# Performance work log

Measured on AMD Instinct MI355X. Metric: run time of the kernel, lower is better.

Reference implementation:

```python
import jax, jax.numpy as jnp
import numpy as np

N_TREES = 10
N_DEPTH = 8
IN_DIM = 2048
CLASSES = 1000
BATCH = 16384
N_DECISION = 2 ** N_DEPTH - 1          # 255
N_LEAF = 2 ** (N_DEPTH + 1)            # 512 (module's own convention)


def _tiling_pattern():
    # Static gather pattern mapping each (leaf, depth) slot to an index into
    # the packed [decision_p, 1 - decision_p] tensor, exactly as in the source.
    tp = np.zeros((N_LEAF, N_DEPTH), dtype=np.int32)
    dec_idx = 0
    for n in range(N_DEPTH):
        j = 0
        for _ in range(2 ** n):
            rep = 2 ** (N_DEPTH - n)
            tp[j:j + rep, n] = dec_idx
            j += rep
            tp[j:j + rep, n] = N_DECISION + dec_idx
            j += rep
            dec_idx += 1
    return tp.reshape(-1)

FLAT_PATTERN = jnp.asarray(_tiling_pattern())  # [N_LEAF * N_DEPTH]


def setup_inputs() -> dict:
    key = jax.random.key(0)
    kx, kd, kl = jax.random.split(key, 3)
    x = jax.random.normal(kx, (BATCH, IN_DIM), dtype=jnp.float32)
    # small scale so sigmoid logits are not fully saturated (mimics uniform init)
    w_d = jax.random.normal(kd, (N_TREES, IN_DIM, N_DECISION), dtype=jnp.float32) * 0.02
    w_l = jax.random.normal(kl, (N_TREES, N_LEAF, CLASSES), dtype=jnp.float32)
    return {"x": x, "w_d": w_d, "w_l": w_l}


def reference(x, w_d, w_l):
    # decision probabilities for all trees: [T, B, N_DECISION]
    decision_p = jax.nn.sigmoid(jnp.einsum('bi,tid->tbd', x, w_d))
    # packed [p, 1-p]: [T, B, 2*N_DECISION]
    pack = jnp.concatenate([decision_p, 1.0 - decision_p], axis=-1)
    # static gather -> path probability factors: [T, B, N_LEAF, N_DEPTH]
    mu = pack[..., FLAT_PATTERN].reshape(N_TREES, x.shape[0], N_LEAF, N_DEPTH)
    leaf_prob = jnp.prod(mu, axis=-1)               # [T, B, N_LEAF]
    leaf_p = jax.nn.softmax(w_l, axis=-1)           # [T, N_LEAF, C]
    # sum over trees, then average
    return jnp.einsum('tbl,tlc->bc', leaf_prob, leaf_p) / N_TREES
```

## Files before the change

kernel.cpp:

```cpp
#include <hip/hip_runtime.h>
#include <stdint.h>

#define T_TREES 10
#define IN_DIM  2048
#define BATCH   16384
#define CLASSES 1000
#define NDEC    255
#define NPAD    256
#define K2DIM   (T_TREES * NPAD)
#define NPADC   1024

typedef unsigned short u16;
typedef float floatx4 __attribute__((ext_vector_type(4)));
typedef __bf16 bf16x8 __attribute__((ext_vector_type(8)));

__device__ __forceinline__ u16 f2bf(float f) {
    union { float f; uint32_t u; } v; v.f = f;
    uint32_t u = v.u;
    return (u16)((u + 0x7FFFu + ((u >> 16) & 1u)) >> 16);
}
__device__ __forceinline__ float bf2f(u16 h) {
    union { uint32_t u; float f; } v; v.u = ((uint32_t)h) << 16;
    return v.f;
}

__device__ __forceinline__ void gld16(u16* lds_p, const u16* g) {
    __builtin_amdgcn_global_load_lds(
        (__attribute__((address_space(1))) const void*)g,
        (__attribute__((address_space(3))) void*)lds_p,
        16, 0, 0);
}

__global__ __launch_bounds__(256) void cast_x_k(const float4* __restrict__ x,
                                                uint2* __restrict__ xb) {
    int i = blockIdx.x * 256 + threadIdx.x;
    float4 v = x[i];
    uint2 o;
    o.x = (uint32_t)f2bf(v.x) | ((uint32_t)f2bf(v.y) << 16);
    o.y = (uint32_t)f2bf(v.z) | ((uint32_t)f2bf(v.w) << 16);
    xb[i] = o;
}

__global__ void transpose_wd_k(const float* __restrict__ wd, u16* __restrict__ wdT) {
    __shared__ float tile[32][33];
    int tx = threadIdx.x, ty = threadIdx.y;
    int t = blockIdx.z;
    int i0 = blockIdx.x * 32, d0 = blockIdx.y * 32;
#pragma unroll
    for (int r = 0; r < 4; ++r) {
        int i = i0 + ty + r * 8;
        int d = d0 + tx;
        float v = (d < NDEC) ? wd[((size_t)t * IN_DIM + i) * NDEC + d] : 0.0f;
        tile[ty + r * 8][tx] = v;
    }
    __syncthreads();
#pragma unroll
    for (int r = 0; r < 4; ++r) {
        int dd = d0 + ty + r * 8;
        int ii = i0 + tx;
        wdT[((size_t)t * NPAD + dd) * IN_DIM + ii] = f2bf(tile[tx][ty + r * 8]);
    }
}

__global__ __launch_bounds__(256) void softmax_fold_k(const float* __restrict__ wl,
                                                      u16* __restrict__ B2) {
    int wid = threadIdx.x >> 6, lane = threadIdx.x & 63;
    int idx = blockIdx.x * 4 + wid;
    int t = idx >> 8, m = idx & 255;
    const float* r0 = wl + ((size_t)t * 512 + 2 * m) * CLASSES;
    const float* r1 = r0 + CLASSES;
    float v0[16], v1[16];
    float mx0 = -3.0e38f, mx1 = -3.0e38f;
#pragma unroll
    for (int j = 0; j < 16; ++j) {
        int c = lane + 64 * j;
        float a = (c < CLASSES) ? r0[c] : -3.0e38f;
        float b = (c < CLASSES) ? r1[c] : -3.0e38f;
        v0[j] = a; v1[j] = b;
        mx0 = fmaxf(mx0, a); mx1 = fmaxf(mx1, b);
    }
#pragma unroll
    for (int o = 32; o > 0; o >>= 1) {
        mx0 = fmaxf(mx0, __shfl_xor(mx0, o));
        mx1 = fmaxf(mx1, __shfl_xor(mx1, o));
    }
    float s0 = 0.f, s1 = 0.f;
#pragma unroll
    for (int j = 0; j < 16; ++j) {
        int c = lane + 64 * j;
        float e0 = (c < CLASSES) ? __expf(v0[j] - mx0) : 0.f;
        float e1 = (c < CLASSES) ? __expf(v1[j] - mx1) : 0.f;
        v0[j] = e0; v1[j] = e1; s0 += e0; s1 += e1;
    }
#pragma unroll
    for (int o = 32; o > 0; o >>= 1) { s0 += __shfl_xor(s0, o); s1 += __shfl_xor(s1, o); }
    float i0 = 0.1f / s0, i1 = 0.1f / s1;
#pragma unroll
    for (int j = 0; j < 16; ++j) {
        int c = lane + 64 * j;
        float v = (c < CLASSES) ? (v0[j] * i0 + v1[j] * i1) : 0.f;
        B2[(size_t)idx * NPADC + c] = f2bf(v);
    }
}

__global__ void transpose_b2_k(const u16* __restrict__ B2, u16* __restrict__ B2t) {
    __shared__ u16 tile[32][33];
    int tx = threadIdx.x, ty = threadIdx.y;
    int k0 = blockIdx.x * 32, c0 = blockIdx.y * 32;
#pragma unroll
    for (int r = 0; r < 4; ++r)
        tile[ty + r * 8][tx] = B2[(size_t)(k0 + ty + r * 8) * NPADC + c0 + tx];
    __syncthreads();
#pragma unroll
    for (int r = 0; r < 4; ++r)
        B2t[(size_t)(c0 + ty + r * 8) * K2DIM + k0 + tx] = tile[tx][ty + r * 8];
}


#define WAITLGKM_(n) asm volatile("s_waitcnt lgkmcnt(" #n ")" ::: "memory")
#define WAITLGKM(n) WAITLGKM_(n)
#define WAITVM_(n) asm volatile("s_waitcnt vmcnt(" #n ")" ::: "memory")
#define WAITVM(n) WAITVM_(n)
#define SB  __builtin_amdgcn_sched_barrier(0)
#define BAR __builtin_amdgcn_s_barrier()

template<int NT, int EPI>
__global__ __launch_bounds__(512, 2) void gemm8p(const u16* __restrict__ A,
                                                 const u16* __restrict__ B,
                                                 void* __restrict__ Cout) {
    constexpr int K = NT * 64;
    __shared__ __align__(16) u16 lds[8 * 8192];

    const int tid  = threadIdx.x;
    const int wid  = tid >> 6;
    const int lane = tid & 63;
    const int wm = wid >> 2, wn = wid & 3;
    const int quad = lane >> 4, t16 = lane & 15;

    const size_t m0 = (size_t)blockIdx.x * 256;
    const size_t n0 = (size_t)blockIdx.y * 256;
    const u16* __restrict__ Ag = A + m0 * (size_t)K;
    const u16* __restrict__ Bg = B + n0 * (size_t)K;

    const uint32_t stOff = (uint32_t)((wid * 8 + (lane >> 3)) * K)
                         + (uint32_t)(((lane & 7) ^ ((lane >> 3) & 7)) * 8);
    const uint32_t stLds = (uint32_t)(wid * 8 * 64);

#define STAGE(slot, o, tk) do { \
    const u16* gp_ = (((o) < 2) ? Bg : Ag) + ((size_t)(((o) & 1) * 128) * K) \
                   + ((size_t)(tk) * 64) + stOff; \
    gld16(&lds[(slot) * 8192 + stLds], gp_); \
    gld16(&lds[(slot) * 8192 + stLds + 4096], gp_ + (size_t)64 * K); \
  } while (0)

#define AOFF(P, mi, kk) (((P) * 4 + 2 + wm) * 8192 + ((mi) * 16 + t16) * 64 \
                         + ((((kk) * 4 + quad) ^ (t16 & 7)) * 8))
#define BOFF(P, ni, kk) (((P) * 4 + ((wn * 64 + (ni) * 16) >> 7)) * 8192 \
                         + (((wn * 64 + (ni) * 16) & 127) + t16) * 64 \
                         + ((((kk) * 4 + quad) ^ (t16 & 7)) * 8))

#define RD2(dst, P, mi0) do { \
    dst[0][0] = *(const bf16x8*)&lds[AOFF(P, (mi0),     0)]; \
    dst[0][1] = *(const bf16x8*)&lds[AOFF(P, (mi0),     1)]; \
    dst[1][0] = *(const bf16x8*)&lds[AOFF(P, (mi0) + 1, 0)]; \
    dst[1][1] = *(const bf16x8*)&lds[AOFF(P, (mi0) + 1, 1)]; \
  } while (0)

#define RDB(dst, P) do { \
    _Pragma("unroll") \
    for (int ni_ = 0; ni_ < 4; ++ni_) { \
      dst[ni_][0] = *(const bf16x8*)&lds[BOFF(P, ni_, 0)]; \
      dst[ni_][1] = *(const bf16x8*)&lds[BOFF(P, ni_, 1)]; \
    } \
  } while (0)

#define MFQ(p, aq, bs) do { \
    _Pragma("unroll") \
    for (int kk_ = 0; kk_ < 2; ++kk_) { \
      _Pragma("unroll") \
      for (int ni_ = 0; ni_ < 4; ++ni_) { \
        acc[2*(p)][ni_]   = __builtin_amdgcn_mfma_f32_16x16x32_bf16( \
            aq[0][kk_], bs[ni_][kk_], acc[2*(p)][ni_], 0, 0, 0); \
        acc[2*(p)+1][ni_] = __builtin_amdgcn_mfma_f32_16x16x32_bf16( \
            aq[1][kk_], bs[ni_][kk_], acc[2*(p)+1][ni_], 0, 0, 0); \
      } \
    } \
  } while (0)

    floatx4 acc[8][4];
#pragma unroll
    for (int i = 0; i < 8; ++i)
#pragma unroll
        for (int j = 0; j < 4; ++j) acc[i][j] = (floatx4){0.f, 0.f, 0.f, 0.f};

    bf16x8 bA[4][2], bB[4][2];
    bf16x8 a0A[2][2], a0B[2][2];
    bf16x8 aT1[2][2], aT2[2][2], aT3[2][2];

    STAGE(0, 0, 0); STAGE(1, 1, 0); STAGE(2, 2, 0); STAGE(3, 3, 0);
    STAGE(4, 0, 1); STAGE(5, 1, 1); STAGE(6, 2, 1);
    WAITVM(6);
    BAR; SB;
    RDB(bA, 0); RD2(a0A, 0, 0);

#define TILE(P, t, S_A1, S_T2, NEXTF, VMN, bcur, bnxt, a0c, a0n) do { \
     \
    RD2(aT1, P, 2); \
    if (S_A1) { STAGE((1 - (P)) * 4 + 3, 3, (t) + 1); } \
    WAITLGKM(4); SB; \
    __builtin_amdgcn_s_setprio(1); MFQ(0, a0c, bcur); __builtin_amdgcn_s_setprio(0); \
    BAR; SB; \
     \
    RD2(aT2, P, 4); RD2(aT3, P, 6); \
    if (S_T2) { STAGE((P) * 4 + 0, 0, (t) + 2); } \
    WAITLGKM(8); SB; \
    __builtin_amdgcn_s_setprio(1); MFQ(1, aT1, bcur); __builtin_amdgcn_s_setprio(0); \
    BAR; SB; \
     \
    if (S_T2) { STAGE((P) * 4 + 1, 1, (t) + 2); } \
    WAITLGKM(0); SB; \
    __builtin_amdgcn_s_setprio(1); MFQ(2, aT2, bcur); __builtin_amdgcn_s_setprio(0); \
    BAR; SB; \
     \
    if (S_T2) { STAGE((P) * 4 + 2, 2, (t) + 2); } \
    if (NEXTF) { WAITVM(VMN); } \
    BAR; SB; \
    if (NEXTF) { RDB(bnxt, 1 - (P)); RD2(a0n, 1 - (P), 0); SB; } \
    __builtin_amdgcn_s_setprio(1); MFQ(3, aT3, bcur); __builtin_amdgcn_s_setprio(0); \
    BAR; SB; \
  } while (0)

    int t = 0;
#pragma unroll 1
    for (int it = 0; it < NT / 2 - 1; ++it, t += 2) {
        TILE(0, t,     true, true, true, 6, bA, bB, a0A, a0B);
        TILE(1, t + 1, true, true, true, 6, bB, bA, a0B, a0A);
    }
    TILE(0, t,     true,  false, true,  0, bA, bB, a0A, a0B);
    TILE(1, t + 1, false, false, false, 0, bB, bA, a0B, a0A);

    if constexpr (EPI == 0) {
        u16* C = (u16*)Cout;
#pragma unroll
        for (int mi = 0; mi < 8; ++mi)
#pragma unroll
            for (int r = 0; r < 4; ++r) {
                const size_t row = m0 + wm * 128 + mi * 16 + quad * 4 + r;
#pragma unroll
                for (int ni = 0; ni < 4; ++ni) {
                    const int col = (int)n0 + wn * 64 + ni * 16 + t16;
                    float v = acc[mi][ni][r];
                    float p = 1.0f / (1.0f + __expf(-v));
                    C[row * (size_t)K2DIM + col] = f2bf(p);
                }
            }
    } else {
        float* C = (float*)Cout;
#pragma unroll
        for (int mi = 0; mi < 8; ++mi)
#pragma unroll
            for (int r = 0; r < 4; ++r) {
                const size_t row = m0 + wm * 128 + mi * 16 + quad * 4 + r;
#pragma unroll
                for (int ni = 0; ni < 4; ++ni) {
                    const int col = (int)n0 + wn * 64 + ni * 16 + t16;
                    if (col < CLASSES)
                        C[row * (size_t)CLASSES + col] = acc[mi][ni][r];
                }
            }
    }
#undef TILE
#undef MFQ
#undef RDB
#undef RD2
#undef BOFF
#undef AOFF
#undef STAGE
}

__global__ __launch_bounds__(256) void leafprod_k(const u16* __restrict__ dp,
                                                  u16* __restrict__ lp) {
    __shared__ float P[4][256];
    int wid = threadIdx.x >> 6, lane = threadIdx.x & 63;
    int idx = blockIdx.x * 4 + wid;
    int t = idx >> 14, b = idx & 16383;
    const u16* row = dp + (size_t)b * K2DIM + t * NPAD;
#pragma unroll
    for (int j = 0; j < 4; ++j)
        P[wid][lane + 64 * j] = bf2f(row[lane + 64 * j]);
    __syncthreads();
#pragma unroll
    for (int j = 0; j < 4; ++j) {
        int m = lane + 64 * j;
        float prod = 1.0f;
#pragma unroll
        for (int n = 0; n < 8; ++n) {
            int dec  = (1 << n) - 1 + (m >> (8 - n));
            int side = (m >> (7 - n)) & 1;
            float p  = P[wid][dec];
            prod *= side ? (1.0f - p) : p;
        }
        lp[(size_t)b * K2DIM + t * NPAD + m] = f2bf(prod);
    }
}

extern "C" void kernel_launch(void* const* d_in, const int* in_sizes, int n_in,
                              void* d_out, int out_size, void* d_ws, size_t ws_size,
                              hipStream_t stream) {
    const float* x   = (const float*)d_in[0];
    const float* w_d = (const float*)d_in[1];
    const float* w_l = (const float*)d_in[2];
    float* out = (float*)d_out;

    char* w = (char*)d_ws;
    u16* B2t = (u16*)w;
    char* region = w + 5242880;
    u16* xb  = (u16*)region;
    u16* wdT = (u16*)(region + 67108864);
    u16* B2  = (u16*)(region + 67108864 + 10485760);
    u16* lp  = (u16*)region;
    u16* dp  = (u16*)(region + 83886080);

    cast_x_k<<<32768, 256, 0, stream>>>((const float4*)x, (uint2*)xb);
    transpose_wd_k<<<dim3(64, 8, T_TREES), dim3(32, 8), 0, stream>>>(w_d, wdT);
    softmax_fold_k<<<640, 256, 0, stream>>>(w_l, B2);
    transpose_b2_k<<<dim3(80, 32), dim3(32, 8), 0, stream>>>(B2, B2t);
    gemm8p<32, 0><<<dim3(64, 10), 512, 0, stream>>>(xb, wdT, dp);
    leafprod_k<<<40960, 256, 0, stream>>>(dp, lp);
    gemm8p<40, 1><<<dim3(64, 4), 512, 0, stream>>>(lp, B2t, out);
}
```

Before: 570.6 us.

## Restructure GEMM main loop into k-split 4x4 MFMA quarters with smaller fragment buffers

Replaces the per-tile schedule of prefetched A/B fragment double-buffers with a simpler four-phase loop. Each phase reads a 4x4 block of A and B fragments for one k-half and issues 16 MFMAs. Global staging is regrouped into pairs (A halves for the next tile, B halves two tiles ahead), and the vmcnt wait depth changes accordingly. This cuts register pressure from the many held fragments, possibly allowing better occupancy or scheduling. In exchange it loses the cross-phase overlap of LDS reads with MFMAs and adds more full barriers and lgkmcnt(0) waits per tile.

```diff
diff --git a/kernel.cpp b/kernel.cpp
--- a/kernel.cpp
+++ b/kernel.cpp
@@ -155,34 +155,31 @@
 
 #define AOFF(P, mi, kk) (((P) * 4 + 2 + wm) * 8192 + ((mi) * 16 + t16) * 64 \
                          + ((((kk) * 4 + quad) ^ (t16 & 7)) * 8))
-#define BOFF(P, ni, kk) (((P) * 4 + ((wn * 64 + (ni) * 16) >> 7)) * 8192 \
-                         + (((wn * 64 + (ni) * 16) & 127) + t16) * 64 \
+#define BOFF(P, ni, kk) (((P) * 4 + (wn >> 1)) * 8192 \
+                         + ((wn & 1) * 64 + (ni) * 16 + t16) * 64 \
                          + ((((kk) * 4 + quad) ^ (t16 & 7)) * 8))
 
-#define RD2(dst, P, mi0) do { \
-    dst[0][0] = *(const bf16x8*)&lds[AOFF(P, (mi0),     0)]; \
-    dst[0][1] = *(const bf16x8*)&lds[AOFF(P, (mi0),     1)]; \
-    dst[1][0] = *(const bf16x8*)&lds[AOFF(P, (mi0) + 1, 0)]; \
-    dst[1][1] = *(const bf16x8*)&lds[AOFF(P, (mi0) + 1, 1)]; \
-  } while (0)
-
-#define RDB(dst, P) do { \
+#define RDA(P, mb, kk) do { \
+    aF[0] = *(const bf16x8*)&lds[AOFF(P, (mb) + 0, kk)]; \
+    aF[1] = *(const bf16x8*)&lds[AOFF(P, (mb) + 1, kk)]; \
+    aF[2] = *(const bf16x8*)&lds[AOFF(P, (mb) + 2, kk)]; \
+    aF[3] = *(const bf16x8*)&lds[AOFF(P, (mb) + 3, kk)]; \
+  } while (0)
+
+#define RDBF(P, kk) do { \
+    bF[0] = *(const bf16x8*)&lds[BOFF(P, 0, kk)]; \
+    bF[1] = *(const bf16x8*)&lds[BOFF(P, 1, kk)]; \
+    bF[2] = *(const bf16x8*)&lds[BOFF(P, 2, kk)]; \
+    bF[3] = *(const bf16x8*)&lds[BOFF(P, 3, kk)]; \
+  } while (0)
+
+#define MF16(mb) do { \
     _Pragma("unroll") \
     for (int ni_ = 0; ni_ < 4; ++ni_) { \
-      dst[ni_][0] = *(const bf16x8*)&lds[BOFF(P, ni_, 0)]; \
-      dst[ni_][1] = *(const bf16x8*)&lds[BOFF(P, ni_, 1)]; \
-    } \
-  } while (0)
-
-#define MFQ(p, aq, bs) do { \
-    _Pragma("unroll") \
-    for (int kk_ = 0; kk_ < 2; ++kk_) { \
       _Pragma("unroll") \
-      for (int ni_ = 0; ni_ < 4; ++ni_) { \
-        acc[2*(p)][ni_]   = __builtin_amdgcn_mfma_f32_16x16x32_bf16( \
-            aq[0][kk_], bs[ni_][kk_], acc[2*(p)][ni_], 0, 0, 0); \
-        acc[2*(p)+1][ni_] = __builtin_amdgcn_mfma_f32_16x16x32_bf16( \
-            aq[1][kk_], bs[ni_][kk_], acc[2*(p)+1][ni_], 0, 0, 0); \
+      for (int j_ = 0; j_ < 4; ++j_) { \
+        acc[(mb) + j_][ni_] = __builtin_amdgcn_mfma_f32_16x16x32_bf16( \
+            aF[j_], bF[ni_], acc[(mb) + j_][ni_], 0, 0, 0); \
       } \
     } \
   } while (0)
@@ -193,51 +190,49 @@
 #pragma unroll
         for (int j = 0; j < 4; ++j) acc[i][j] = (floatx4){0.f, 0.f, 0.f, 0.f};
 
-    bf16x8 bA[4][2], bB[4][2];
-    bf16x8 a0A[2][2], a0B[2][2];
-    bf16x8 aT1[2][2], aT2[2][2], aT3[2][2];
+    bf16x8 aF[4], bF[4];
 
     STAGE(0, 0, 0); STAGE(1, 1, 0); STAGE(2, 2, 0); STAGE(3, 3, 0);
-    STAGE(4, 0, 1); STAGE(5, 1, 1); STAGE(6, 2, 1);
-    WAITVM(6);
-    BAR; SB;
-    RDB(bA, 0); RD2(a0A, 0, 0);
-
-#define TILE(P, t, S_A1, S_T2, NEXTF, VMN, bcur, bnxt, a0c, a0n) do { \
+    STAGE(4, 0, 1); STAGE(5, 1, 1);
+    WAITVM(4);
+    BAR;
+
+#define TILE(P, t, SA, SBG, HASW, WN) do { \
      \
-    RD2(aT1, P, 2); \
-    if (S_A1) { STAGE((1 - (P)) * 4 + 3, 3, (t) + 1); } \
-    WAITLGKM(4); SB; \
-    __builtin_amdgcn_s_setprio(1); MFQ(0, a0c, bcur); __builtin_amdgcn_s_setprio(0); \
-    BAR; SB; \
+    RDA(P, 0, 0); RDBF(P, 0); \
+    if (SA) { STAGE((1 - (P)) * 4 + 2, 2, (t) + 1); \
+              STAGE((1 - (P)) * 4 + 3, 3, (t) + 1); } \
+    BAR; WAITLGKM(0); SB; \
+    __builtin_amdgcn_s_setprio(1); MF16(0); __builtin_amdgcn_s_setprio(0); \
+    BAR; \
      \
-    RD2(aT2, P, 4); RD2(aT3, P, 6); \
-    if (S_T2) { STAGE((P) * 4 + 0, 0, (t) + 2); } \
-    WAITLGKM(8); SB; \
-    __builtin_amdgcn_s_setprio(1); MFQ(1, aT1, bcur); __builtin_amdgcn_s_setprio(0); \
-    BAR; SB; \
+    RDA(P, 4, 0); \
+    BAR; WAITLGKM(0); SB; \
+    __builtin_amdgcn_s_setprio(1); MF16(4); __builtin_amdgcn_s_setprio(0); \
+    BAR; \
      \
-    if (S_T2) { STAGE((P) * 4 + 1, 1, (t) + 2); } \
-    WAITLGKM(0); SB; \
-    __builtin_amdgcn_s_setprio(1); MFQ(2, aT2, bcur); __builtin_amdgcn_s_setprio(0); \
-    BAR; SB; \
+    RDA(P, 0, 1); RDBF(P, 1); \
+    BAR; WAITLGKM(0); SB; \
+    __builtin_amdgcn_s_setprio(1); MF16(0); __builtin_amdgcn_s_setprio(0); \
+    BAR; \
      \
-    if (S_T2) { STAGE((P) * 4 + 2, 2, (t) + 2); } \
-    if (NEXTF) { WAITVM(VMN); } \
-    BAR; SB; \
-    if (NEXTF) { RDB(bnxt, 1 - (P)); RD2(a0n, 1 - (P), 0); SB; } \
-    __builtin_amdgcn_s_setprio(1); MFQ(3, aT3, bcur); __builtin_amdgcn_s_setprio(0); \
-    BAR; SB; \
+    RDA(P, 4, 1); \
+    if (SBG) { STAGE((P) * 4 + 0, 0, (t) + 2); \
+               STAGE((P) * 4 + 1, 1, (t) + 2); } \
+    if (HASW) { WAITVM(WN); } \
+    BAR; WAITLGKM(0); SB; \
+    __builtin_amdgcn_s_setprio(1); MF16(4); __builtin_amdgcn_s_setprio(0); \
+    BAR; \
   } while (0)
 
     int t = 0;
 #pragma unroll 1
     for (int it = 0; it < NT / 2 - 1; ++it, t += 2) {
-        TILE(0, t,     true, true, true, 6, bA, bB, a0A, a0B);
-        TILE(1, t + 1, true, true, true, 6, bB, bA, a0B, a0A);
-    }
-    TILE(0, t,     true,  false, true,  0, bA, bB, a0A, a0B);
-    TILE(1, t + 1, false, false, false, 0, bB, bA, a0B, a0A);
+        TILE(0, t,     true, true, true, 4);
+        TILE(1, t + 1, true, true, true, 4);
+    }
+    TILE(0, NT - 2, true,  false, true,  0);
+    TILE(1, NT - 1, false, false, false, 0);
 
     if constexpr (EPI == 0) {
         u16* C = (u16*)Cout;
@@ -270,9 +265,9 @@
             }
     }
 #undef TILE
-#undef MFQ
-#undef RDB
-#undef RD2
+#undef MF16
+#undef RDBF
+#undef RDA
 #undef BOFF
 #undef AOFF
 #undef STAGE
```

After: 522.5 us. 8.4% less time.
